# Optimization experiments

Measured on AMD Instinct MI355X. Metric: run time of the kernel, lower is better.

## Reference

```python
import jax, jax.numpy as jnp
import numpy as np

HIDDEN, BATCH, SEQ, LAYERS = 256, 32, 1024, 4


def setup_inputs() -> dict:
    key = jax.random.key(0)
    ks = jax.random.split(key, 6)
    NE = HIDDEN * BATCH
    return {
        "h_data": jax.random.normal(ks[0], ((SEQ + 1) * LAYERS * NE,), dtype=jnp.float32),
        "x_data": jax.random.normal(ks[1], (SEQ * (LAYERS + 1) * NE,), dtype=jnp.float32),
        "c_data": jax.random.normal(ks[2], ((SEQ + 1) * LAYERS * NE,), dtype=jnp.float32),
        "W": jax.random.normal(ks[3], (LAYERS, 4 * HIDDEN, HIDDEN), dtype=jnp.float32) * 0.05,
        "R": jax.random.normal(ks[4], (LAYERS, 4 * HIDDEN, HIDDEN), dtype=jnp.float32) * 0.05,
        "bias": jax.random.normal(ks[5], (LAYERS, 4 * HIDDEN), dtype=jnp.float32) * 0.05,
        "hiddenSize": HIDDEN,
        "miniBatch": BATCH,
        "seqLength": SEQ,
        "numLayers": LAYERS,
    }


def reference(h_data, x_data, c_data, W, R, bias, hiddenSize, miniBatch, seqLength, numLayers):
    NE = hiddenSize * miniBatch
    # inter-layer workspace in the CUDA code; here they are produced by scan).
    x = x_data[: seqLength * NE].reshape(seqLength, miniBatch, hiddenSize)
    h0 = h_data.reshape(numLayers, seqLength + 1, miniBatch, hiddenSize)[:, 0]
    c0 = c_data.reshape(numLayers, seqLength + 1, miniBatch, hiddenSize)[:, 0]

    inp = x
    for l in range(numLayers):
        Wl, Rl, bl = W[l], R[l], bias[l]

        def step(carry, xt, Wl=Wl, Rl=Rl, bl=bl):
            h, c = carry
            gates = xt @ Wl.T + h @ Rl.T + bl            # [B, 4H]
            i, f, g, o = jnp.split(gates, 4, axis=-1)
            i = jax.nn.sigmoid(i)
            f = jax.nn.sigmoid(f)
            g = jnp.tanh(g)
            o = jax.nn.sigmoid(o)
            c_new = f * c + i * g
            h_new = o * jnp.tanh(c_new)
            return (h_new, c_new), h_new

        _, inp = jax.lax.scan(step, (h0[l], c0[l]), inp)
    # Top-layer hidden states for all timesteps: [seqLength, miniBatch, hiddenSize]
    return inp
```

## Files before the change

kernel.cpp:

```cpp
#include <hip/hip_runtime.h>


#define HID  256
#define BAT  32
#define SEQL 1024
#define NLAY 4
#define NE   (HID*BAT)
#define WGPL 32
#define GSTR 36

typedef __attribute__((ext_vector_type(8))) short bf16x8;
typedef __attribute__((ext_vector_type(4))) float f32x4;

union U8 { bf16x8 v; unsigned short s[8]; unsigned u[4]; };

__device__ __forceinline__ unsigned short bf16_rne(float f) {
    unsigned u = __float_as_uint(f);
    u += 0x7FFFu + ((u >> 16) & 1u);
    return (unsigned short)(u >> 16);
}
__device__ __forceinline__ float bf16_to_f(unsigned short h) {
    return __uint_as_float(((unsigned)h) << 16);
}
__device__ __forceinline__ unsigned pack_hl(float f) {
    unsigned short hi = bf16_rne(f);
    unsigned short lo = bf16_rne(f - bf16_to_f(hi));
    return (((unsigned)hi) << 16) | lo;
}

__device__ __forceinline__ uint4 ld_cohx4(const unsigned* p) {
    uint4 r;
    asm volatile("global_load_dwordx4 %0, %1, off sc0 sc1" : "=v"(r) : "v"(p) : "memory");
    return r;
}
__device__ __forceinline__ void st_coh(unsigned* p, unsigned v) {
    asm volatile("global_store_dword %0, %1, off sc0 sc1" :: "v"(p), "v"(v) : "memory");
}
__device__ __forceinline__ void waitcnt0() {
    asm volatile("s_waitcnt vmcnt(0)" ::: "memory");
}

__device__ __forceinline__ float sigm(float x)  { return 1.0f / (1.0f + __expf(-x)); }
__device__ __forceinline__ float tanhx(float x) { return 1.0f - 2.0f / (__expf(2.0f * x) + 1.0f); }

__global__ __launch_bounds__(256) void pack_x(unsigned* xp) {
    int i = (blockIdx.x * 256 + threadIdx.x) * 4;
    float4 f = *(const float4*)((const float*)xp + i);
    uint4 u;
    u.x = pack_hl(f.x); u.y = pack_hl(f.y);
    u.z = pack_hl(f.z); u.w = pack_hl(f.w);
    *(uint4*)(xp + i) = u;
}

__global__ __launch_bounds__(256, 1)
void lstm_mfma(unsigned* __restrict__ hslab,
               const float* __restrict__ c_data,
               const float* __restrict__ W,
               const float* __restrict__ R,
               const float* __restrict__ bias,
               const unsigned* __restrict__ xpack,
               float* __restrict__ out,
               int* __restrict__ flags)
{
    __shared__ float ldsg[32 * GSTR];

    const int tid  = threadIdx.x;
    const int bx   = blockIdx.x;
    const int l    = bx >> 5;
    const int w    = bx & 31;

    const int wv   = tid >> 6;
    const int lane = tid & 63;
    const int mh   = wv & 1;
    const int nh   = wv >> 1;
    const int ln15 = lane & 15;
    const int kq   = lane >> 4;

    const int n_loc = nh * 16 + ln15;
    const int gate  = n_loc >> 3;
    const int uu    = n_loc & 7;
    const int grow  = gate * HID + w * 8 + uu;
    const int bg    = mh * 16 + ln15;

    bf16x8 Bhi[16], Blo[16];
    {
        const float* Wl = W + (size_t)l * 4 * HID * HID;
        const float* Rl = R + (size_t)l * 4 * HID * HID;
        #pragma unroll
        for (int s = 0; s < 16; ++s) {
            int k0 = s * 32 + kq * 8;
            const float* src = (k0 < HID) ? (Wl + (size_t)grow * HID + k0)
                                          : (Rl + (size_t)grow * HID + (k0 - HID));
            float4 f0 = *(const float4*)src;
            float4 f1 = *(const float4*)(src + 4);
            float ff[8] = {f0.x, f0.y, f0.z, f0.w, f1.x, f1.y, f1.z, f1.w};
            U8 hi, lo;
            #pragma unroll
            for (int j = 0; j < 8; ++j) {
                hi.s[j] = bf16_rne(ff[j]);
                lo.s[j] = bf16_rne(ff[j] - bf16_to_f(hi.s[j]));
            }
            Bhi[s] = hi.v; Blo[s] = lo.v;
        }
    }

    const float bias_n = bias[l * 4 * HID + grow];

    const int uu2 = tid >> 5;
    const int b2  = tid & 31;
    float cst = c_data[(size_t)l * (SEQL + 1) * NE + b2 * HID + w * 8 + uu2];

    unsigned* hbuf = hslab;
    const float* h0f = (const float*)hslab + (size_t)l * (SEQL + 1) * NE;

    for (int t = 0; t < SEQL; ++t) {
        if (tid == 0) {
            if (t > 0)
                while (__hip_atomic_load(&flags[l * SEQL + t - 1],
                       __ATOMIC_RELAXED, __HIP_MEMORY_SCOPE_AGENT) < WGPL)
                    __builtin_amdgcn_s_sleep(1);
            if (l > 0)
                while (__hip_atomic_load(&flags[(l - 1) * SEQL + t],
                       __ATOMIC_RELAXED, __HIP_MEMORY_SCOPE_AGENT) < WGPL)
                    __builtin_amdgcn_s_sleep(1);
        }
        __syncthreads();

        const unsigned* xsrc = (l == 0)
            ? (xpack + (size_t)t * NE)
            : (hbuf + ((size_t)(l - 1) * (SEQL + 1) + (t + 1)) * NE);

        uint4 araw[32];
        if (t > 0) {
            const unsigned* hsrc = hbuf + ((size_t)l * (SEQL + 1) + t) * NE;
            #pragma unroll
            for (int s = 0; s < 16; ++s) {
                const unsigned* p = (s < 8)
                    ? (xsrc + bg * HID + s * 32 + kq * 8)
                    : (hsrc + bg * HID + (s - 8) * 32 + kq * 8);
                araw[2 * s]     = ld_cohx4(p);
                araw[2 * s + 1] = ld_cohx4(p + 4);
            }
            asm volatile("s_waitcnt vmcnt(16)" ::: "memory");
        } else {
            #pragma unroll
            for (int s = 0; s < 8; ++s) {
                const unsigned* p = xsrc + bg * HID + s * 32 + kq * 8;
                araw[2 * s]     = ld_cohx4(p);
                araw[2 * s + 1] = ld_cohx4(p + 4);
            }
            #pragma unroll
            for (int s = 8; s < 16; ++s) {
                const float* hp = h0f + bg * HID + (s - 8) * 32 + kq * 8;
                float4 f0 = *(const float4*)hp;
                float4 f1 = *(const float4*)(hp + 4);
                uint4 a0, a1;
                a0.x = pack_hl(f0.x); a0.y = pack_hl(f0.y);
                a0.z = pack_hl(f0.z); a0.w = pack_hl(f0.w);
                a1.x = pack_hl(f1.x); a1.y = pack_hl(f1.y);
                a1.z = pack_hl(f1.z); a1.w = pack_hl(f1.w);
                araw[2 * s] = a0; araw[2 * s + 1] = a1;
            }
            waitcnt0();
        }

        f32x4 acc0 = {bias_n, bias_n, bias_n, bias_n};
        f32x4 acc1 = {0.f, 0.f, 0.f, 0.f};
        f32x4 acc2 = {0.f, 0.f, 0.f, 0.f};
        #pragma unroll
        for (int s = 0; s < 16; ++s) {
            if (s == 8 && t > 0) waitcnt0();
            uint4 d0 = araw[2 * s], d1 = araw[2 * s + 1];
            U8 ahi, alo;
            ahi.u[0] = __builtin_amdgcn_perm(d0.y, d0.x, 0x07060302u);
            ahi.u[1] = __builtin_amdgcn_perm(d0.w, d0.z, 0x07060302u);
            ahi.u[2] = __builtin_amdgcn_perm(d1.y, d1.x, 0x07060302u);
            ahi.u[3] = __builtin_amdgcn_perm(d1.w, d1.z, 0x07060302u);
            alo.u[0] = __builtin_amdgcn_perm(d0.y, d0.x, 0x05040100u);
            alo.u[1] = __builtin_amdgcn_perm(d0.w, d0.z, 0x05040100u);
            alo.u[2] = __builtin_amdgcn_perm(d1.y, d1.x, 0x05040100u);
            alo.u[3] = __builtin_amdgcn_perm(d1.w, d1.z, 0x05040100u);
            acc0 = __builtin_amdgcn_mfma_f32_16x16x32_bf16(ahi.v, Bhi[s], acc0, 0, 0, 0);
            acc1 = __builtin_amdgcn_mfma_f32_16x16x32_bf16(ahi.v, Blo[s], acc1, 0, 0, 0);
            acc2 = __builtin_amdgcn_mfma_f32_16x16x32_bf16(alo.v, Bhi[s], acc2, 0, 0, 0);
        }
        f32x4 cc = acc0 + acc1;
        cc = cc + acc2;

        *(f32x4*)&ldsg[n_loc * GSTR + mh * 16 + kq * 4] = cc;
        __syncthreads();

        {
            float gi = ldsg[(0 * 8 + uu2) * GSTR + b2];
            float gf = ldsg[(1 * 8 + uu2) * GSTR + b2];
            float gg = ldsg[(2 * 8 + uu2) * GSTR + b2];
            float go = ldsg[(3 * 8 + uu2) * GSTR + b2];
            float iv = sigm(gi), fv = sigm(gf), gv = tanhx(gg), ov = sigm(go);
            cst = fv * cst + iv * gv;
            float hv = ov * tanhx(cst);
            unsigned dw = pack_hl(hv);
            unsigned* dst = hbuf + ((size_t)l * (SEQL + 1) + (t + 1)) * NE
                          + b2 * HID + w * 8 + uu2;
            st_coh(dst, dw);
            if (l == NLAY - 1)
                out[(size_t)t * NE + b2 * HID + w * 8 + uu2] = hv;
        }
        waitcnt0();
        __syncthreads();

        if (tid == 0)
            __hip_atomic_fetch_add(&flags[l * SEQL + t], 1,
                                   __ATOMIC_RELAXED, __HIP_MEMORY_SCOPE_AGENT);
    }
}

extern "C" void kernel_launch(void* const* d_in, const int* in_sizes, int n_in,
                              void* d_out, int out_size, void* d_ws, size_t ws_size,
                              hipStream_t stream) {
    unsigned*    h_data = (unsigned*)d_in[0];
    unsigned*    x_data = (unsigned*)d_in[1];
    float*       c_data = (float*)d_in[2];
    const float* W      = (const float*)d_in[3];
    const float* R      = (const float*)d_in[4];
    const float* bias   = (const float*)d_in[5];
    float* out = (float*)d_out;

    const size_t flag_bytes = (size_t)NLAY * SEQL * sizeof(int);
    int* flags;
    if (ws_size >= flag_bytes) flags = (int*)d_ws;
    else                       flags = (int*)(c_data + NE);
    hipMemsetAsync(flags, 0, flag_bytes, stream);

    pack_x<<<dim3(8192), dim3(256), 0, stream>>>(x_data);

    lstm_mfma<<<dim3(NLAY * WGPL), dim3(256), 0, stream>>>(
        h_data, c_data, W, R, bias, x_data, out, flags);
}
```

Baseline: 6.557 ms.

## Replace per-step counter flags with per-workgroup progress counters polled by a wave

Each workgroup now bumps its own monotonically increasing progress counter instead of a shared per-timestep counter that all 32 groups atomically increment. A full wave polls all 32 counters of the current and previous layer in parallel and checks them with a wave-wide vote, so the shared-counter contention and the serial two-loop wait are removed. Layer-0 input loads are issued before the wait, and the top-layer output store is moved after the flag release so it sits off the critical path. The change relies on relaxed atomics and coherent loads still providing the required ordering.

```diff
diff --git a/kernel.cpp b/kernel.cpp
--- a/kernel.cpp
+++ b/kernel.cpp
@@ -81,6 +81,12 @@
     const int uu    = n_loc & 7;
     const int grow  = gate * HID + w * 8 + uu;
     const int bg    = mh * 16 + ln15;
+
+    const int pl = lane & 31;
+    const int* fpoll = (lane < 32) ? (flags + l * 32 + pl)
+                     : ((l > 0)    ? (flags + (l - 1) * 32 + pl)
+                                   : (flags + pl));
+    const int thr_base = (lane < 32) ? 0 : ((l > 0) ? 1 : -0x40000000);
 
     bf16x8 Bhi[16], Blo[16];
     {
@@ -114,30 +120,45 @@
     const float* h0f = (const float*)hslab + (size_t)l * (SEQL + 1) * NE;
 
     for (int t = 0; t < SEQL; ++t) {
-        if (tid == 0) {
-            if (t > 0)
-                while (__hip_atomic_load(&flags[l * SEQL + t - 1],
-                       __ATOMIC_RELAXED, __HIP_MEMORY_SCOPE_AGENT) < WGPL)
-                    __builtin_amdgcn_s_sleep(1);
-            if (l > 0)
-                while (__hip_atomic_load(&flags[(l - 1) * SEQL + t],
-                       __ATOMIC_RELAXED, __HIP_MEMORY_SCOPE_AGENT) < WGPL)
-                    __builtin_amdgcn_s_sleep(1);
-        }
-        __syncthreads();
-
         const unsigned* xsrc = (l == 0)
             ? (xpack + (size_t)t * NE)
             : (hbuf + ((size_t)(l - 1) * (SEQL + 1) + (t + 1)) * NE);
 
         uint4 araw[32];
+
+        if (l == 0 && t > 0) {
+            #pragma unroll
+            for (int s = 0; s < 8; ++s) {
+                const unsigned* p = xsrc + bg * HID + s * 32 + kq * 8;
+                araw[2 * s]     = ld_cohx4(p);
+                araw[2 * s + 1] = ld_cohx4(p + 4);
+            }
+        }
+
+        if (wv == 0) {
+            const int thr = thr_base + t;
+            for (;;) {
+                int v = __hip_atomic_load(fpoll, __ATOMIC_RELAXED,
+                                          __HIP_MEMORY_SCOPE_AGENT);
+                if (__all(v >= thr)) break;
+                __builtin_amdgcn_s_sleep(1);
+            }
+        }
+        __syncthreads();
+
         if (t > 0) {
             const unsigned* hsrc = hbuf + ((size_t)l * (SEQL + 1) + t) * NE;
-            #pragma unroll
-            for (int s = 0; s < 16; ++s) {
-                const unsigned* p = (s < 8)
-                    ? (xsrc + bg * HID + s * 32 + kq * 8)
-                    : (hsrc + bg * HID + (s - 8) * 32 + kq * 8);
+            if (l > 0) {
+                #pragma unroll
+                for (int s = 0; s < 8; ++s) {
+                    const unsigned* p = xsrc + bg * HID + s * 32 + kq * 8;
+                    araw[2 * s]     = ld_cohx4(p);
+                    araw[2 * s + 1] = ld_cohx4(p + 4);
+                }
+            }
+            #pragma unroll
+            for (int s = 8; s < 16; ++s) {
+                const unsigned* p = hsrc + bg * HID + (s - 8) * 32 + kq * 8;
                 araw[2 * s]     = ld_cohx4(p);
                 araw[2 * s + 1] = ld_cohx4(p + 4);
             }
@@ -190,6 +211,7 @@
         *(f32x4*)&ldsg[n_loc * GSTR + mh * 16 + kq * 4] = cc;
         __syncthreads();
 
+        float hv;
         {
             float gi = ldsg[(0 * 8 + uu2) * GSTR + b2];
             float gf = ldsg[(1 * 8 + uu2) * GSTR + b2];
@@ -197,20 +219,21 @@
             float go = ldsg[(3 * 8 + uu2) * GSTR + b2];
             float iv = sigm(gi), fv = sigm(gf), gv = tanhx(gg), ov = sigm(go);
             cst = fv * cst + iv * gv;
-            float hv = ov * tanhx(cst);
+            hv = ov * tanhx(cst);
             unsigned dw = pack_hl(hv);
             unsigned* dst = hbuf + ((size_t)l * (SEQL + 1) + (t + 1)) * NE
                           + b2 * HID + w * 8 + uu2;
             st_coh(dst, dw);
-            if (l == NLAY - 1)
-                out[(size_t)t * NE + b2 * HID + w * 8 + uu2] = hv;
         }
         waitcnt0();
         __syncthreads();
 
         if (tid == 0)
-            __hip_atomic_fetch_add(&flags[l * SEQL + t], 1,
+            __hip_atomic_fetch_add(&flags[l * 32 + w], 1,
                                    __ATOMIC_RELAXED, __HIP_MEMORY_SCOPE_AGENT);
+
+        if (l == NLAY - 1)
+            out[(size_t)t * NE + b2 * HID + w * 8 + uu2] = hv;
     }
 }
 
@@ -225,7 +248,7 @@
     const float* bias   = (const float*)d_in[5];
     float* out = (float*)d_out;
 
-    const size_t flag_bytes = (size_t)NLAY * SEQL * sizeof(int);
+    const size_t flag_bytes = (size_t)NLAY * WGPL * sizeof(int);
     int* flags;
     if (ws_size >= flag_bytes) flags = (int*)d_ws;
     else                       flags = (int*)(c_data + NE);
```

Result: slower. 6.805 ms (+3.8%).
